# Kernel optimization log

Hardware: AMD Instinct MI355X
Metric: run time of the kernel (lower is better)

## Reference

```python
import jax, jax.numpy as jnp
import numpy as np
from jax import lax

THRESH = 0.5
DECAY = 0.2
LENS = 0.5

@jax.custom_vjp
def act_fun(x):
    return (x > THRESH).astype(x.dtype)

def _act_fwd(x):
    return act_fun(x), x

def _act_bwd(x, g):
    return (g * (jnp.abs(x - THRESH) < LENS).astype(g.dtype),)

act_fun.defvjp(_act_fwd, _act_bwd)

def conv2d(x, w, b, stride):
    y = lax.conv_general_dilated(x, w, (stride, stride), 'VALID',
                                 dimension_numbers=('NCHW', 'OIHW', 'NCHW'))
    return y + b[None, :, None, None]

def setup_inputs() -> dict:
    key = jax.random.key(0)
    ks = jax.random.split(key, 7)
    B = 32
    std = float(np.sqrt(3.0 / (8 * 16)))
    data = jax.random.uniform(ks[0], (B, 1, 28, 28), dtype=jnp.float32)
    conv_w = jax.random.normal(ks[1], (256, 1, 9, 9), dtype=jnp.float32) * float(np.sqrt(1.0 / 81))
    conv_b = jax.random.normal(ks[2], (256,), dtype=jnp.float32) * 0.01
    prim_w = jax.random.normal(ks[3], (256, 256, 9, 9), dtype=jnp.float32) * float(np.sqrt(1.0 / (256 * 81)))
    prim_b = jax.random.normal(ks[4], (256,), dtype=jnp.float32) * 0.01
    W = jax.random.normal(ks[5], (1152, 10, 16, 8), dtype=jnp.float32) * std
    bias = jax.random.normal(ks[6], (16, 1), dtype=jnp.float32) * std
    return {"data": data, "conv_w": conv_w, "conv_b": conv_b,
            "prim_w": prim_w, "prim_b": prim_b, "W": W, "bias": bias,
            "time_window": 5}

def capsnet_forward(data, conv_w, conv_b, prim_w, prim_b, W, bias, time_window):
    B = data.shape[0]
    R, C, O = 1152, 10, 16  # num_routes, num_capsules, out_channels
    f32 = jnp.float32
    conv_mem = conv_spike = jnp.zeros((B, 256, 20, 20), f32)
    prim_mem = prim_spike = jnp.zeros((B, R, 8), f32)
    dig_mem = dig_spike = jnp.zeros((B, R, C, O), f32)
    dig2_mem = dig2_spike = jnp.zeros((B, C, O), f32)
    out_mem = jnp.zeros((B, C, O), f32)
    trace_u = jnp.zeros((B, R, C, O), f32)
    b_ij = jnp.ones((1, R, C), f32) / R  # [1,1152,10] (trailing 1 dim dropped)
    decay_tr = jnp.exp(jnp.asarray(-1.0 / 1.5, f32))

    for _ in range(time_window):
        # conv layer membrane update
        conv_out = jax.nn.relu(conv2d(data, conv_w, conv_b, 1))  # [B,256,20,20]
        conv_mem = (conv_mem - conv_spike * THRESH) * DECAY + conv_out
        conv_spike = act_fun(conv_mem)
        # primary caps: 8 parallel convs fused into one (out chans 8*32), then view [B,1152,8]
        prim_out = conv2d(conv_spike, prim_w, prim_b, 2).reshape(B, R, 8)
        prim_mem = (prim_mem - prim_spike * THRESH) * DECAY + prim_out
        prim_spike = act_fun(prim_mem)
        # digit caps: u_hat = W @ x + bias  -> [B,R,C,O]
        u_hat = jnp.einsum('rcoi,bri->brco', W, prim_spike) + bias[:, 0]
        dig_mem = (dig_mem - dig_spike * THRESH) * DECAY + u_hat
        dig_spike = act_fun(dig_mem)
        # digit caps 2: routing-weighted sum over routes
        s_j = jnp.einsum('rc,brco->bco', b_ij[0], dig_spike)  # [B,C,O]
        dig2_mem = (dig2_mem - dig2_spike * THRESH) * DECAY + s_j
        dig2_spike = act_fun(dig2_mem)
        out_mem = out_mem + s_j
        # training-time b_ij / trace update (no_grad in torch)
        ds = lax.stop_gradient(dig_spike)
        d2s = lax.stop_gradient(dig2_spike)
        b_ij = jnp.clip(b_ij, -0.05, 1.0)
        trace_u = jnp.where(ds != 0, 1.0, trace_u * decay_tr)
        delta = 0.0008 * jnp.einsum('brco,bco->brc', trace_u - 0.1, d2s).mean(axis=0)
        b_ij = lax.stop_gradient(b_ij + delta[None])

    output = out_mem / time_window          # [B,10,16]
    classes = jnp.sqrt((output ** 2).sum(2))  # Decoder -> [B,10]
    return classes

def reference(data, conv_w, conv_b, prim_w, prim_b, W, bias, time_window):
    return capsnet_forward(data, conv_w, conv_b, prim_w, prim_b, W, bias, time_window)
```

## Files before the change

kernel.cpp:

```cpp
#include <hip/hip_runtime.h>
#include <stdint.h>

#define THRESH 0.5f
#define DECAY  0.2f
#define TSTEPS 5

#define B_        32
#define CONV_ELEMS (32*256*20*20)
#define RR        1152
#define CC        10
#define PRIM_ELEMS (32*1152*8)
#define DIG_ELEMS  (32*1152*160)
#define MM        256
#define NN        1152
#define KK        20736
#define KSPLIT    18
#define NCH64     18
#define NGG       324

typedef __attribute__((ext_vector_type(4))) int   int32x4;
typedef __attribute__((ext_vector_type(4))) float f32x4;

__device__ __forceinline__ void async16(void* l, const void* g) {
    __builtin_amdgcn_global_load_lds(
        (const __attribute__((address_space(1))) uint32_t*)g,
        (__attribute__((address_space(3))) uint32_t*)l, 16, 0, 0);
}

__global__ void k_init_bij(float* bij) {
    int i = blockIdx.x * 256 + threadIdx.x;
    if (i < RR * CC) bij[i] = 1.0f / 1152.0f;
}

__global__ __launch_bounds__(256) void k_absmax(const float* __restrict__ w,
                                                unsigned* __restrict__ out) {
    __shared__ float sm[4];
    const f32x4* w4 = (const f32x4*)w;
    float m = 0.f;
    for (int i = blockIdx.x * 256 + threadIdx.x; i < MM * KK / 4; i += 256 * 256) {
        f32x4 v = w4[i];
        m = fmaxf(m, fmaxf(fmaxf(fabsf(v.x), fabsf(v.y)),
                           fmaxf(fabsf(v.z), fabsf(v.w))));
    }
    #pragma unroll
    for (int off = 1; off < 64; off <<= 1)
        m = fmaxf(m, __shfl_xor(m, off));
    int lane = threadIdx.x & 63, wv = threadIdx.x >> 6;
    if (lane == 0) sm[wv] = m;
    __syncthreads();
    if (threadIdx.x == 0) {
        float r = fmaxf(fmaxf(sm[0], sm[1]), fmaxf(sm[2], sm[3]));
        atomicMax(out, __float_as_uint(r));
    }
}

__global__ __launch_bounds__(320) void k_conv1(const float* __restrict__ data,
                                               const float* __restrict__ cw,
                                               const float* __restrict__ cb,
                                               float* __restrict__ out) {
    __shared__ float sdat[784];
    __shared__ float swt[1296];
    __shared__ float sout[20 * 333];
    int b = blockIdx.x, og = blockIdx.y;
    int tid = threadIdx.x;
    for (int i = tid; i < 196; i += 320)
        ((f32x4*)sdat)[i] = ((const f32x4*)(data + b * 784))[i];
    for (int i = tid; i < 324; i += 320)
        ((f32x4*)swt)[i] = ((const f32x4*)(cw + og * 1296))[i];
    __syncthreads();
    int ocl = tid / 20, y = tid % 20;
    float acc[20];
    #pragma unroll
    for (int x = 0; x < 20; ++x) acc[x] = 0.f;
    const float* wb = &swt[ocl * 81];
    #pragma unroll
    for (int ky = 0; ky < 9; ++ky) {
        const float* dr = &sdat[(y + ky) * 28];
        float d[28];
        #pragma unroll
        for (int t4 = 0; t4 < 7; ++t4) {
            f32x4 v = ((const f32x4*)dr)[t4];
            d[t4 * 4 + 0] = v.x; d[t4 * 4 + 1] = v.y;
            d[t4 * 4 + 2] = v.z; d[t4 * 4 + 3] = v.w;
        }
        float w[9];
        #pragma unroll
        for (int q = 0; q < 9; ++q) w[q] = wb[ky * 9 + q];
        #pragma unroll
        for (int kx = 0; kx < 9; ++kx)
            #pragma unroll
            for (int x = 0; x < 20; ++x)
                acc[x] += d[x + kx] * w[kx];
    }
    float bias = cb[og * 16 + ocl];
    #pragma unroll
    for (int x = 0; x < 20; ++x)
        sout[y * 333 + x * 16 + ocl] = fmaxf(acc[x] + bias, 0.f);
    __syncthreads();
    const size_t base = (size_t)b * 102400 + og * 16;
    for (int f = tid; f < 6400; f += 320) {
        int yy = f / 320, rem = f % 320;
        out[base + (size_t)(f >> 4) * 256 + (f & 15)] = sout[yy * 333 + rem];
    }
}

__global__ __launch_bounds__(256) void k_wsplit(const float* __restrict__ w,
                                                signed char* __restrict__ A2,
                                                const unsigned* __restrict__ mb) {
    int t = blockIdx.x * 256 + threadIdx.x;
    if (t >= 16 * NGG * 64) return;
    float inv = 32512.f / fmaxf(__uint_as_float(mb[0]), 1e-30f);
    int lane = t & 63;
    int rest = t >> 6;
    int gg = rest % NGG;
    int rowblk = rest / NGG;
    int row = rowblk * 16 + (lane & 15);
    int k0 = gg * 64 + (lane >> 4) * 16;
    union { signed char b[16]; int32x4 v; } H, L;
    #pragma unroll
    for (int j = 0; j < 16; ++j) {
        int k = k0 + j;
        int kw = k >> 8, ic = k & 255;
        float f = w[((size_t)row * 256 + ic) * 81 + kw];
        int q = (int)lrintf(f * inv);
        int lo = (int)(signed char)(q & 0xFF);
        int hi = (q - lo) >> 8;
        H.b[j] = (signed char)hi;
        L.b[j] = (signed char)lo;
    }
    size_t base = ((size_t)(rowblk * NGG + gg) * 2) * 1024 + lane * 16;
    *(int32x4*)(A2 + base)        = H.v;
    *(int32x4*)(A2 + base + 1024) = L.v;
}

__device__ __forceinline__ void convmem_body(int i, float* mem, const float* cout,
                                             unsigned char* spk) {
    f32x4 m = ((f32x4*)mem)[i];
    f32x4 c = ((const f32x4*)cout)[i];
    unsigned pv = 0;
    #pragma unroll
    for (int j = 0; j < 4; ++j) {
        float mv = m[j];
        float ps = (mv > THRESH) ? THRESH : 0.f;
        mv = (mv - ps) * DECAY + c[j];
        m[j] = mv;
        if (mv > THRESH) pv |= (1u << (8 * j));
    }
    ((f32x4*)mem)[i] = m;
    ((unsigned*)spk)[i] = pv;
}

__global__ void k_convmem(float* __restrict__ mem, const float* __restrict__ cout,
                          unsigned char* __restrict__ spk) {
    int i = blockIdx.x * 256 + threadIdx.x;
    if (i >= CONV_ELEMS / 4) return;
    convmem_body(i, mem, cout, spk);
}

__device__ __forceinline__ void bij_body(int g, const uint8_t* __restrict__ age,
                                         const float* __restrict__ d2mem,
                                         float* __restrict__ bij) {
    int r = g / 160, co = g % 160, c = co / 16, o = co & 15;
    const float dtr = expf(-1.0f / 1.5f);
    float tab[5];
    tab[0] = 1.f;
    #pragma unroll
    for (int k = 1; k < 5; ++k) tab[k] = tab[k - 1] * dtr;
    float acc = 0.f;
    #pragma unroll 8
    for (int b = 0; b < B_; ++b) {
        uint8_t a = age[(size_t)b * (RR * 160) + g];
        float tv = (a == 0 || a > 5) ? 0.f : tab[a - 1];
        float d2 = (d2mem[b * 160 + co] > THRESH) ? 1.f : 0.f;
        acc += (tv - 0.1f) * d2;
    }
    #pragma unroll
    for (int off = 1; off < 16; off <<= 1) acc += __shfl_xor(acc, off);
    if (o == 0) {
        float bo = bij[r * 10 + c];
        bo = fminf(fmaxf(bo, -0.05f), 1.0f);
        bij[r * 10 + c] = bo + 0.0008f * (acc * (1.0f / 32.0f));
    }
}

__global__ __launch_bounds__(256) void k_gemm(const signed char* __restrict__ A2,
                                              const unsigned char* __restrict__ spk,
                                              const unsigned* __restrict__ mb,
                                              float* __restrict__ Cp,
                                              int do_bij,
                                              const uint8_t* __restrict__ age,
                                              const float* __restrict__ d2mem,
                                              float* __restrict__ bij) {
    __shared__ signed char sB[3][128 * 64];
    int bid = blockIdx.x;
    int tid = threadIdx.x;
    if (bid >= 648) {
        if (!do_bij) return;
        int g = (bid - 648) * 256 + tid;
        bij_body(g, age, d2mem, bij);
        return;
    }
    int slot = bid & 7, j = bid >> 3;
    int tm = slot & 3, kpar = slot >> 2;
    int tn = j / 9, ks2 = j % 9;
    int ks = ks2 * 2 + kpar;

    int rbB[2], slB[2];
    #pragma unroll
    for (int p = 0; p < 2; ++p) {
        int f = p * 256 + tid;
        int n = f >> 2;
        slB[p] = (f & 3) ^ (n & 3) ^ ((n >> 2) & 3);
        int gn = tn * 128 + n;
        int b = gn / 36, pos = gn % 36;
        rbB[p] = ((b * 20 + (pos / 6) * 2) * 20 + (pos % 6) * 2) * 256;
    }

    int wid = tid >> 6, lane = tid & 63;
    int wr = wid >> 1, wc = wid & 1;
    int fr = lane & 15, sl = lane >> 4;

    const signed char* pA[2][2];
    #pragma unroll
    for (int d = 0; d < 2; ++d)
        #pragma unroll
        for (int i = 0; i < 2; ++i) {
            int blk = tm * 4 + wr * 2 + i;
            pA[d][i] = A2 + ((size_t)((blk * NGG + ks * NCH64) * 2 + d)) * 1024 + lane * 16;
        }

    int offB[4];
    #pragma unroll
    for (int jj = 0; jj < 4; ++jj) {
        int n = wc * 64 + jj * 16 + fr;
        offB[jj] = n * 64 + ((sl ^ (n & 3) ^ ((n >> 2) & 3)) << 4);
    }

#define STAGE(buf, c) do {                                                       \
        _Pragma("unroll")                                                        \
        for (int p = 0; p < 2; ++p) {                                            \
            int kp_ = ks * 1152 + (c) * 64 + slB[p] * 16;                        \
            int kw_ = kp_ >> 8, ic_ = kp_ & 255;                                 \
            async16(&sB[buf][(p * 256 + tid) * 16],                              \
                    spk + rbB[p] + ((kw_ / 9) * 20 + (kw_ % 9)) * 256 + ic_);    \
        }                                                                        \
    } while (0)

#define LOADA(dst, c) do {                                                       \
        _Pragma("unroll")                                                        \
        for (int d = 0; d < 2; ++d)                                              \
            _Pragma("unroll")                                                    \
            for (int i = 0; i < 2; ++i)                                          \
                dst[d][i] = *(const int32x4*)(pA[d][i] + (size_t)(c) * 2048);    \
    } while (0)

#define ITER(c, CUR, NXT) do {                                                   \
        asm volatile("s_waitcnt vmcnt(6)" ::: "memory");                         \
        __builtin_amdgcn_s_barrier();                                            \
        if ((c) + 2 < NCH64) STAGE(((c) + 2) % 3, (c) + 2);                      \
        if ((c) + 1 < NCH64) LOADA(NXT, (c) + 1);                                \
        int32x4 bv[4];                                                           \
        const signed char* sbc = sB[(c) % 3];                                    \
        _Pragma("unroll")                                                        \
        for (int jj = 0; jj < 4; ++jj) bv[jj] = *(const int32x4*)&sbc[offB[jj]]; \
        _Pragma("unroll")                                                        \
        for (int i = 0; i < 2; ++i)                                              \
            _Pragma("unroll")                                                    \
            for (int jj = 0; jj < 4; ++jj) {                                     \
                accH[i][jj] = __builtin_amdgcn_mfma_i32_16x16x64_i8(             \
                    CUR[0][i], bv[jj], accH[i][jj], 0, 0, 0);                    \
                accL[i][jj] = __builtin_amdgcn_mfma_i32_16x16x64_i8(             \
                    CUR[1][i], bv[jj], accL[i][jj], 0, 0, 0);                    \
            }                                                                    \
    } while (0)

    int32x4 accH[2][4] = {};
    int32x4 accL[2][4] = {};
    int32x4 aA[2][2], aB[2][2];
    STAGE(0, 0);
    STAGE(1, 1);
    LOADA(aA, 0);
    for (int c = 0; c < NCH64; c += 2) {
        ITER(c, aA, aB);
        ITER(c + 1, aB, aA);
    }
#undef ITER
#undef LOADA
#undef STAGE

    float s1 = fmaxf(__uint_as_float(mb[0]), 1e-30f) / 32512.f;
    float s256 = s1 * 256.f;
    int colb = lane & 15, rb4 = (lane >> 4) * 4;
    float* Co = Cp + (size_t)ks * (MM * NN);
    #pragma unroll
    for (int i = 0; i < 2; ++i)
        #pragma unroll
        for (int jj = 0; jj < 4; ++jj) {
            int gm = tm * 64 + wr * 32 + i * 16 + rb4;
            int gn = tn * 128 + wc * 64 + jj * 16 + colb;
            #pragma unroll
            for (int q = 0; q < 4; ++q)
                Co[(size_t)(gm + q) * NN + gn] =
                    (float)accH[i][jj][q] * s256 + (float)accL[i][jj][q] * s1;
        }
}

__global__ __launch_bounds__(320) void k_dig(const float* __restrict__ Cp,
                                             const float* __restrict__ pb,
                                             float* __restrict__ pmem,
                                             const float* __restrict__ W,
                                             const float* __restrict__ bias,
                                             const float* __restrict__ bij,
                                             float* __restrict__ dmem,
                                             uint8_t* __restrict__ age,
                                             float* __restrict__ sjp) {
    __shared__ float ps[128];
    int r0 = blockIdx.x * 4;
    int by = blockIdx.y;
    int tid = threadIdx.x;
    if (tid < 128) {
        int bl = tid >> 5, ff = tid & 31;
        int f = r0 * 8 + ff;
        int oc = f / 36, pos = f % 36;
        int b = by * 4 + bl;
        int n = b * 36 + pos;
        float sacc = pb[oc];
        #pragma unroll
        for (int kss = 0; kss < KSPLIT; ++kss)
            sacc += Cp[(size_t)kss * (MM * NN) + oc * NN + n];
        size_t pidx = (size_t)b * 9216 + f;
        float m = pmem[pidx];
        float pso = (m > THRESH) ? THRESH : 0.f;
        m = (m - pso) * DECAY + sacc;
        pmem[pidx] = m;
        ps[(ff >> 3) * 32 + bl * 8 + (ff & 7)] = (m > THRESH) ? 1.f : 0.f;
    }
    __syncthreads();
    int co = tid % 160, bh = tid / 160;
    int c = co >> 4, o = co & 15;
    float bo = bias[o];

    size_t idx8[4][2];
    float  m8[4][2];
    uint8_t a8[4][2];
    #pragma unroll
    for (int r = 0; r < 4; ++r)
        #pragma unroll
        for (int bb = 0; bb < 2; ++bb) {
            int bl = bh * 2 + bb;
            idx8[r][bb] = ((size_t)((by * 4 + bl) * 1152 + r0 + r)) * 160 + co;
            m8[r][bb] = dmem[idx8[r][bb]];
            a8[r][bb] = age[idx8[r][bb]];
        }

    float sacc2[2] = {0.f, 0.f};
    #pragma unroll
    for (int r = 0; r < 4; ++r) {
        int rr = r0 + r;
        const float* wp = W + ((size_t)((rr * 10 + c) * 16 + o)) * 8;
        f32x4 w0 = *(const f32x4*)wp;
        f32x4 w1 = *(const f32x4*)(wp + 4);
        float bv = bij[rr * 10 + c];
        #pragma unroll
        for (int bb = 0; bb < 2; ++bb) {
            const float* p8 = &ps[r * 32 + (bh * 2 + bb) * 8];
            f32x4 pa = *(const f32x4*)p8;
            f32x4 pc = *(const f32x4*)(p8 + 4);
            float u = bo + w0.x * pa.x + w0.y * pa.y + w0.z * pa.z + w0.w * pa.w
                         + w1.x * pc.x + w1.y * pc.y + w1.z * pc.z + w1.w * pc.w;
            float m = m8[r][bb];
            float psv = (m > THRESH) ? THRESH : 0.f;
            m = (m - psv) * DECAY + u;
            dmem[idx8[r][bb]] = m;
            bool sp = m > THRESH;
            if (sp) sacc2[bb] += bv;
            uint8_t a = a8[r][bb];
            age[idx8[r][bb]] = sp ? (uint8_t)1 : (a ? (uint8_t)(a + 1) : (uint8_t)0);
        }
    }
    size_t pbase = ((size_t)(by * 288 + blockIdx.x)) * 640;
    #pragma unroll
    for (int bb = 0; bb < 2; ++bb)
        sjp[pbase + (bh * 2 + bb) * 160 + co] = sacc2[bb];
}

__global__ void k_dig2a(const float* __restrict__ sjp, float* __restrict__ sjp2) {
    int e = blockIdx.x * 256 + threadIdx.x;
    int b = e / 160, co = e % 160;
    int y = b >> 2, rem = (b & 3) * 160 + co;
    int x0 = blockIdx.y * 24;
    float a = 0.f;
    #pragma unroll 8
    for (int x = x0; x < x0 + 24; ++x)
        a += sjp[((size_t)(y * 288 + x)) * 640 + rem];
    sjp2[blockIdx.y * 5120 + e] = a;
}

__global__ void k_mix(const float* __restrict__ sjp2, float* __restrict__ d2mem,
                      float* __restrict__ omem, float* __restrict__ cmem,
                      const float* __restrict__ cout, unsigned char* __restrict__ spk) {
    int bx = blockIdx.x;
    int tid = threadIdx.x;
    if (bx < 20) {
        int e = bx * 256 + tid;
        float s = 0.f;
        #pragma unroll
        for (int k = 0; k < 12; ++k) s += sjp2[k * 5120 + e];
        float m = d2mem[e];
        float ps = (m > THRESH) ? THRESH : 0.f;
        d2mem[e] = (m - ps) * DECAY + s;
        omem[e] += s;
    } else {
        int i = (bx - 20) * 256 + tid;
        if (i < CONV_ELEMS / 4) convmem_body(i, cmem, cout, spk);
    }
}

__global__ void k_out(const float* __restrict__ omem, float* __restrict__ out) {
    int i = blockIdx.x * 64 + threadIdx.x;
    if (i >= B_ * CC) return;
    int b = i / 10, c = i % 10;
    float s = 0.f;
    #pragma unroll
    for (int o = 0; o < 16; ++o) {
        float v = omem[b * 160 + c * 16 + o] / 5.0f;
        s += v * v;
    }
    out[i] = sqrtf(s);
}

extern "C" void kernel_launch(void* const* d_in, const int* in_sizes, int n_in,
                              void* d_out, int out_size, void* d_ws, size_t ws_size,
                              hipStream_t stream) {
    const float* data   = (const float*)d_in[0];
    const float* conv_w = (const float*)d_in[1];
    const float* conv_b = (const float*)d_in[2];
    const float* prim_w = (const float*)d_in[3];
    const float* prim_b = (const float*)d_in[4];
    const float* W      = (const float*)d_in[5];
    const float* bias   = (const float*)d_in[6];
    float* out = (float*)d_out;

    char* ws = (char*)d_ws;
    size_t off = 0;
    auto alloc = [&](size_t bytes) {
        void* p = ws + off;
        off = (off + bytes + 255) & ~(size_t)255;
        return p;
    };
    size_t zbase = off;
    float*          conv_mem = (float*)alloc((size_t)CONV_ELEMS * 4);
    float*          prim_mem = (float*)alloc((size_t)PRIM_ELEMS * 4);
    float*          dig_mem  = (float*)alloc((size_t)DIG_ELEMS * 4);
    float*          dig2_mem = (float*)alloc(5120 * 4);
    float*          out_mem  = (float*)alloc(5120 * 4);
    uint8_t*        age      = (uint8_t*)alloc(DIG_ELEMS);
    unsigned*       mb       = (unsigned*)alloc(256);
    size_t zbytes = off - zbase;
    float*          conv_out = (float*)alloc((size_t)CONV_ELEMS * 4);
    unsigned char*  conv_spk = (unsigned char*)alloc((size_t)CONV_ELEMS);
    float*          sjp      = (float*)alloc((size_t)2304 * 640 * 4);
    float*          sjp2     = (float*)alloc((size_t)12 * 5120 * 4);
    float*          bij      = (float*)alloc(RR * CC * 4);
    signed char*    A2       = (signed char*)alloc((size_t)MM * KK * 2);
    float*          Cp       = (float*)alloc((size_t)KSPLIT * MM * NN * 4);

    hipMemsetAsync(ws + zbase, 0, zbytes, stream);

    k_init_bij<<<(RR * CC + 255) / 256, 256, 0, stream>>>(bij);
    k_absmax<<<256, 256, 0, stream>>>(prim_w, mb);
    k_conv1<<<dim3(32, 16), 320, 0, stream>>>(data, conv_w, conv_b, conv_out);
    k_wsplit<<<(16 * NGG * 64 + 255) / 256, 256, 0, stream>>>(prim_w, A2, mb);
    k_convmem<<<(CONV_ELEMS / 4 + 255) / 256, 256, 0, stream>>>(conv_mem, conv_out, conv_spk);

    for (int t = 0; t < TSTEPS; ++t) {
        int do_bij = (t > 0);
        int ggrid = 648 + (do_bij ? 720 : 0);
        k_gemm<<<ggrid, 256, 0, stream>>>(A2, conv_spk, mb, Cp, do_bij, age, dig2_mem, bij);
        k_dig<<<dim3(288, 8), 320, 0, stream>>>(Cp, prim_b, prim_mem, W, bias, bij, dig_mem, age, sjp);
        k_dig2a<<<dim3(20, 12), 256, 0, stream>>>(sjp, sjp2);
        int mgrid = 20 + ((t < TSTEPS - 1) ? (CONV_ELEMS / 4 + 255) / 256 : 0);
        k_mix<<<mgrid, 256, 0, stream>>>(sjp2, dig2_mem, out_mem, conv_mem, conv_out, conv_spk);
    }
    k_out<<<(B_ * CC + 63) / 64, 64, 0, stream>>>(out_mem, out);
}
```

Before: 373.7 us.

## Precompute all conv spikes once and reduce split-K GEMM with integer atomics

Because the conv input is identical every timestep, all five conv spike maps are computed up front in one kernel, which removes the per-step conv membrane pass and its fp32 state traffic. The split-K GEMM partials are no longer written as 18 float slabs for k_dig to sum. Each tile instead atomically adds its combined int32 accumulator into a single integer buffer, and scaling moves into k_dig. The buffer is re-zeroed inside k_dig2a. Integer atomics keep the sum exact, but they add atomic contention and need the extra zeroing step.

```diff
diff --git a/kernel.cpp b/kernel.cpp
--- a/kernel.cpp
+++ b/kernel.cpp
@@ -133,28 +133,24 @@
     *(int32x4*)(A2 + base + 1024) = L.v;
 }
 
-__device__ __forceinline__ void convmem_body(int i, float* mem, const float* cout,
-                                             unsigned char* spk) {
-    f32x4 m = ((f32x4*)mem)[i];
-    f32x4 c = ((const f32x4*)cout)[i];
-    unsigned pv = 0;
-    #pragma unroll
-    for (int j = 0; j < 4; ++j) {
-        float mv = m[j];
-        float ps = (mv > THRESH) ? THRESH : 0.f;
-        mv = (mv - ps) * DECAY + c[j];
-        m[j] = mv;
-        if (mv > THRESH) pv |= (1u << (8 * j));
-    }
-    ((f32x4*)mem)[i] = m;
-    ((unsigned*)spk)[i] = pv;
-}
-
-__global__ void k_convmem(float* __restrict__ mem, const float* __restrict__ cout,
-                          unsigned char* __restrict__ spk) {
+__global__ void k_convall(const float* __restrict__ cout, unsigned char* __restrict__ spk5) {
     int i = blockIdx.x * 256 + threadIdx.x;
     if (i >= CONV_ELEMS / 4) return;
-    convmem_body(i, mem, cout, spk);
+    f32x4 c = ((const f32x4*)cout)[i];
+    f32x4 m = {0.f, 0.f, 0.f, 0.f};
+    #pragma unroll
+    for (int t = 0; t < TSTEPS; ++t) {
+        unsigned pv = 0;
+        #pragma unroll
+        for (int j = 0; j < 4; ++j) {
+            float mv = m[j];
+            float ps = (mv > THRESH) ? THRESH : 0.f;
+            mv = (mv - ps) * DECAY + c[j];
+            m[j] = mv;
+            if (mv > THRESH) pv |= (1u << (8 * j));
+        }
+        ((unsigned*)(spk5 + (size_t)t * CONV_ELEMS))[i] = pv;
+    }
 }
 
 __device__ __forceinline__ void bij_body(int g, const uint8_t* __restrict__ age,
@@ -185,8 +181,7 @@
 
 __global__ __launch_bounds__(256) void k_gemm(const signed char* __restrict__ A2,
                                               const unsigned char* __restrict__ spk,
-                                              const unsigned* __restrict__ mb,
-                                              float* __restrict__ Cp,
+                                              int* __restrict__ Ci,
                                               int do_bij,
                                               const uint8_t* __restrict__ age,
                                               const float* __restrict__ d2mem,
@@ -288,10 +283,7 @@
 #undef LOADA
 #undef STAGE
 
-    float s1 = fmaxf(__uint_as_float(mb[0]), 1e-30f) / 32512.f;
-    float s256 = s1 * 256.f;
     int colb = lane & 15, rb4 = (lane >> 4) * 4;
-    float* Co = Cp + (size_t)ks * (MM * NN);
     #pragma unroll
     for (int i = 0; i < 2; ++i)
         #pragma unroll
@@ -300,12 +292,13 @@
             int gn = tn * 128 + wc * 64 + jj * 16 + colb;
             #pragma unroll
             for (int q = 0; q < 4; ++q)
-                Co[(size_t)(gm + q) * NN + gn] =
-                    (float)accH[i][jj][q] * s256 + (float)accL[i][jj][q] * s1;
-        }
-}
-
-__global__ __launch_bounds__(320) void k_dig(const float* __restrict__ Cp,
+                atomicAdd(&Ci[(size_t)(gm + q) * NN + gn],
+                          accH[i][jj][q] * 256 + accL[i][jj][q]);
+        }
+}
+
+__global__ __launch_bounds__(320) void k_dig(const int* __restrict__ Ci,
+                                             const unsigned* __restrict__ mb,
                                              const float* __restrict__ pb,
                                              float* __restrict__ pmem,
                                              const float* __restrict__ W,
@@ -319,15 +312,13 @@
     int by = blockIdx.y;
     int tid = threadIdx.x;
     if (tid < 128) {
+        float s1 = fmaxf(__uint_as_float(mb[0]), 1e-30f) / 32512.f;
         int bl = tid >> 5, ff = tid & 31;
         int f = r0 * 8 + ff;
         int oc = f / 36, pos = f % 36;
         int b = by * 4 + bl;
         int n = b * 36 + pos;
-        float sacc = pb[oc];
-        #pragma unroll
-        for (int kss = 0; kss < KSPLIT; ++kss)
-            sacc += Cp[(size_t)kss * (MM * NN) + oc * NN + n];
+        float sacc = pb[oc] + (float)Ci[(size_t)oc * NN + n] * s1;
         size_t pidx = (size_t)b * 9216 + f;
         float m = pmem[pidx];
         float pso = (m > THRESH) ? THRESH : 0.f;
@@ -384,36 +375,39 @@
         sjp[pbase + (bh * 2 + bb) * 160 + co] = sacc2[bb];
 }
 
-__global__ void k_dig2a(const float* __restrict__ sjp, float* __restrict__ sjp2) {
-    int e = blockIdx.x * 256 + threadIdx.x;
-    int b = e / 160, co = e % 160;
-    int y = b >> 2, rem = (b & 3) * 160 + co;
-    int x0 = blockIdx.y * 24;
-    float a = 0.f;
-    #pragma unroll 8
-    for (int x = x0; x < x0 + 24; ++x)
-        a += sjp[((size_t)(y * 288 + x)) * 640 + rem];
-    sjp2[blockIdx.y * 5120 + e] = a;
-}
-
-__global__ void k_mix(const float* __restrict__ sjp2, float* __restrict__ d2mem,
-                      float* __restrict__ omem, float* __restrict__ cmem,
-                      const float* __restrict__ cout, unsigned char* __restrict__ spk) {
+__global__ void k_dig2a(const float* __restrict__ sjp, float* __restrict__ sjp2,
+                        int* __restrict__ Ci) {
     int bx = blockIdx.x;
     int tid = threadIdx.x;
-    if (bx < 20) {
-        int e = bx * 256 + tid;
-        float s = 0.f;
-        #pragma unroll
-        for (int k = 0; k < 12; ++k) s += sjp2[k * 5120 + e];
-        float m = d2mem[e];
-        float ps = (m > THRESH) ? THRESH : 0.f;
-        d2mem[e] = (m - ps) * DECAY + s;
-        omem[e] += s;
+    if (bx < 240) {
+        int gx = bx % 20, ky = bx / 20;
+        int e = gx * 256 + tid;
+        int b = e / 160, co = e % 160;
+        int y = b >> 2, rem = (b & 3) * 160 + co;
+        int x0 = ky * 24;
+        float a = 0.f;
+        #pragma unroll 8
+        for (int x = x0; x < x0 + 24; ++x)
+            a += sjp[((size_t)(y * 288 + x)) * 640 + rem];
+        sjp2[ky * 5120 + e] = a;
     } else {
-        int i = (bx - 20) * 256 + tid;
-        if (i < CONV_ELEMS / 4) convmem_body(i, cmem, cout, spk);
-    }
+        int idx = (bx - 240) * 256 + tid;
+        int32x4 z = {0, 0, 0, 0};
+        ((int32x4*)Ci)[idx] = z;
+    }
+}
+
+__global__ void k_dig2b(const float* __restrict__ sjp2, float* __restrict__ d2mem,
+                        float* __restrict__ omem) {
+    int e = blockIdx.x * 256 + threadIdx.x;
+    if (e >= B_ * 160) return;
+    float s = 0.f;
+    #pragma unroll
+    for (int k = 0; k < 12; ++k) s += sjp2[k * 5120 + e];
+    float m = d2mem[e];
+    float ps = (m > THRESH) ? THRESH : 0.f;
+    d2mem[e] = (m - ps) * DECAY + s;
+    omem[e] += s;
 }
 
 __global__ void k_out(const float* __restrict__ omem, float* __restrict__ out) {
@@ -449,21 +443,20 @@
         return p;
     };
     size_t zbase = off;
-    float*          conv_mem = (float*)alloc((size_t)CONV_ELEMS * 4);
     float*          prim_mem = (float*)alloc((size_t)PRIM_ELEMS * 4);
     float*          dig_mem  = (float*)alloc((size_t)DIG_ELEMS * 4);
     float*          dig2_mem = (float*)alloc(5120 * 4);
     float*          out_mem  = (float*)alloc(5120 * 4);
     uint8_t*        age      = (uint8_t*)alloc(DIG_ELEMS);
     unsigned*       mb       = (unsigned*)alloc(256);
+    int*            Ci       = (int*)alloc((size_t)MM * NN * 4);
     size_t zbytes = off - zbase;
     float*          conv_out = (float*)alloc((size_t)CONV_ELEMS * 4);
-    unsigned char*  conv_spk = (unsigned char*)alloc((size_t)CONV_ELEMS);
+    unsigned char*  spk5     = (unsigned char*)alloc((size_t)TSTEPS * CONV_ELEMS);
     float*          sjp      = (float*)alloc((size_t)2304 * 640 * 4);
     float*          sjp2     = (float*)alloc((size_t)12 * 5120 * 4);
     float*          bij      = (float*)alloc(RR * CC * 4);
     signed char*    A2       = (signed char*)alloc((size_t)MM * KK * 2);
-    float*          Cp       = (float*)alloc((size_t)KSPLIT * MM * NN * 4);
 
     hipMemsetAsync(ws + zbase, 0, zbytes, stream);
 
@@ -471,16 +464,17 @@
     k_absmax<<<256, 256, 0, stream>>>(prim_w, mb);
     k_conv1<<<dim3(32, 16), 320, 0, stream>>>(data, conv_w, conv_b, conv_out);
     k_wsplit<<<(16 * NGG * 64 + 255) / 256, 256, 0, stream>>>(prim_w, A2, mb);
-    k_convmem<<<(CONV_ELEMS / 4 + 255) / 256, 256, 0, stream>>>(conv_mem, conv_out, conv_spk);
+    k_convall<<<(CONV_ELEMS / 4 + 255) / 256, 256, 0, stream>>>(conv_out, spk5);
 
     for (int t = 0; t < TSTEPS; ++t) {
         int do_bij = (t > 0);
         int ggrid = 648 + (do_bij ? 720 : 0);
-        k_gemm<<<ggrid, 256, 0, stream>>>(A2, conv_spk, mb, Cp, do_bij, age, dig2_mem, bij);
-        k_dig<<<dim3(288, 8), 320, 0, stream>>>(Cp, prim_b, prim_mem, W, bias, bij, dig_mem, age, sjp);
-        k_dig2a<<<dim3(20, 12), 256, 0, stream>>>(sjp, sjp2);
-        int mgrid = 20 + ((t < TSTEPS - 1) ? (CONV_ELEMS / 4 + 255) / 256 : 0);
-        k_mix<<<mgrid, 256, 0, stream>>>(sjp2, dig2_mem, out_mem, conv_mem, conv_out, conv_spk);
+        k_gemm<<<ggrid, 256, 0, stream>>>(A2, spk5 + (size_t)t * CONV_ELEMS, Ci,
+                                          do_bij, age, dig2_mem, bij);
+        k_dig<<<dim3(288, 8), 320, 0, stream>>>(Ci, mb, prim_b, prim_mem, W, bias,
+                                                bij, dig_mem, age, sjp);
+        k_dig2a<<<528, 256, 0, stream>>>(sjp, sjp2, Ci);
+        k_dig2b<<<20, 256, 0, stream>>>(sjp2, dig2_mem, out_mem);
     }
     k_out<<<(B_ * CC + 63) / 64, 64, 0, stream>>>(out_mem, out);
 }
```

After: 367.5 us (median of 2 runs). Within noise of the previous version (-1.7%).
